# Optimization experiments

Measured on AMD Instinct MI355X. Metric: run time of the kernel, lower is better.

The kernel has to match this reference:

```python
import jax, jax.numpy as jnp
import numpy as np

EPS = 1e-08

def setup_inputs() -> dict:
    key = jax.random.key(0)
    k1, k2, k3, k4 = jax.random.split(key, 4)
    B, T, D, D_sample = 16, 512, 2048, 4096
    z_hist = jax.random.normal(k1, (B, T, D), dtype=jnp.float32)
    decay_rates = jax.random.normal(k2, (D_sample,), dtype=jnp.float32)
    idx_i = jax.random.randint(k3, (D_sample,), 0, D)
    idx_j = jax.random.randint(k4, (D_sample,), 0, D)
    return {"z_hist": z_hist, "decay_rates": decay_rates, "idx_i": idx_i, "idx_j": idx_j}

def reference(z_hist, decay_rates, idx_i, idx_j):
    B, T, D = z_hist.shape
    r = jax.nn.softplus(decay_rates)                      # [N]
    times = jnp.arange(T, dtype=z_hist.dtype)             # [T]
    # decay[t, n] = exp(-r_n * (T - 1 - t))
    decay = jnp.exp(-r[None, :] * (T - 1 - times)[:, None])  # [T, N]
    z_i = z_hist[:, :, idx_i]                              # [B, T, N]
    z_j = z_hist[:, :, idx_j]                              # [B, T, N]
    num = jnp.einsum('btn,btn,tn->bn', z_i, z_j, decay)    # [B, N]
    den = jnp.sqrt(decay.sum(axis=0) + EPS)                # [N]
    return num / den[None, :]
```

## Files before the change

### kernel.cpp

```cpp
#include <hip/hip_runtime.h>
#include <hip/hip_bf16.h>
#include <math.h>

#define B_   16
#define T_   512
#define D_   2048
#define DS_  4096
#define TCHUNK 8
#define EPS_ 1e-8f


__global__ __launch_bounds__(256) void pre_kernel(const float* __restrict__ decay_rates,
                                                  float* __restrict__ num,
                                                  float* __restrict__ inv_den,
                                                  float* __restrict__ neg_r,
                                                  float* __restrict__ er) {
    int gtid = blockIdx.x * 256 + threadIdx.x;
    num[gtid] = 0.f;
    if (gtid < DS_) {
        float x = decay_rates[gtid];
        float r  = (x > 20.f) ? x : log1pf(expf(x));
        float nr = -r;
        float s = 0.f;
        for (int k = 0; k < T_; ++k) s += expf(nr * (float)k);
        inv_den[gtid] = 1.0f / sqrtf(s + EPS_);
        neg_r[gtid]   = nr;
        er[gtid]      = expf(r);
    }
}

__global__ __launch_bounds__(256) void main_kernel(const float* __restrict__ z,
                                                   const int* __restrict__ idx_i,
                                                   const int* __restrict__ idx_j,
                                                   const float* __restrict__ neg_r,
                                                   const float* __restrict__ er,
                                                   float* __restrict__ num) {
    __shared__ float rows[TCHUNK * D_];
    const int tc  = blockIdx.x;
    const int b   = blockIdx.y;
    const int tid = threadIdx.x;

    const float4* src4 = reinterpret_cast<const float4*>(z + ((size_t)b * T_ + (size_t)tc * TCHUNK) * D_);
    float4* lds4 = reinterpret_cast<float4*>(rows);
    #pragma unroll
    for (int v = 0; v < (TCHUNK * D_ / 4) / 256; ++v)
        lds4[tid + v * 256] = src4[tid + v * 256];
    __syncthreads();

    const int kbase = (T_ - 1) - tc * TCHUNK;

    #pragma unroll 1
    for (int s = 0; s < DS_ / 256; ++s) {
        const int n  = tid + s * 256;
        const int ii = idx_i[n];
        const int jj = idx_j[n];
        float w = __expf(neg_r[n] * (float)kbase);
        const float g = er[n];
        float acc = 0.f;
        #pragma unroll
        for (int tl = 0; tl < TCHUNK; ++tl) {
            acc += rows[tl * D_ + ii] * rows[tl * D_ + jj] * w;
            w *= g;
        }
        atomicAdd(&num[b * DS_ + n], acc);
    }
}

__global__ __launch_bounds__(256) void fin_kernel(const float* __restrict__ num,
                                                  const float* __restrict__ inv_den,
                                                  float* __restrict__ out) {
    int gtid = blockIdx.x * 256 + threadIdx.x;
    out[gtid] = num[gtid] * inv_den[gtid & (DS_ - 1)];
}

extern "C" void kernel_launch(void* const* d_in, const int* in_sizes, int n_in,
                              void* d_out, int out_size, void* d_ws, size_t ws_size,
                              hipStream_t stream) {
    const float* z  = (const float*)d_in[0];
    const float* dr = (const float*)d_in[1];
    const int*   ii = (const int*)d_in[2];
    const int*   jj = (const int*)d_in[3];
    float* out = (float*)d_out;

    float* num     = (float*)d_ws;
    float* inv_den = num + B_ * DS_;
    float* neg_r   = inv_den + DS_;
    float* er      = neg_r + DS_;

    hipLaunchKernelGGL(pre_kernel, dim3((B_ * DS_) / 256), dim3(256), 0, stream,
                       dr, num, inv_den, neg_r, er);
    hipLaunchKernelGGL(main_kernel, dim3(T_ / TCHUNK, B_), dim3(256), 0, stream,
                       z, ii, jj, neg_r, er, num);
    hipLaunchKernelGGL(fin_kernel, dim3((B_ * DS_) / 256), dim3(256), 0, stream,
                       num, inv_den, out);
}
```

Measured before the change: 137.1 us.

## Transpose time chunk into float4 LDS quads, halve TCHUNK, closed-form decay sum

```diff
diff --git a/kernel.cpp b/kernel.cpp
--- a/kernel.cpp
+++ b/kernel.cpp
@@ -6,7 +6,7 @@
 #define T_   512
 #define D_   2048
 #define DS_  4096
-#define TCHUNK 8
+#define TCHUNK 4
 #define EPS_ 1e-8f
 
 
@@ -19,49 +19,50 @@
     num[gtid] = 0.f;
     if (gtid < DS_) {
         float x = decay_rates[gtid];
-        float r  = (x > 20.f) ? x : log1pf(expf(x));
-        float nr = -r;
-        float s = 0.f;
-        for (int k = 0; k < T_; ++k) s += expf(nr * (float)k);
-        inv_den[gtid] = 1.0f / sqrtf(s + EPS_);
-        neg_r[gtid]   = nr;
+        float r = (x > 20.f) ? x : log1pf(expf(x));
+        float S = expm1f(-r * (float)T_) / expm1f(-r);
+        inv_den[gtid] = 1.0f / sqrtf(S + EPS_);
+        neg_r[gtid]   = -r;
         er[gtid]      = expf(r);
     }
 }
 
-__global__ __launch_bounds__(256) void main_kernel(const float* __restrict__ z,
-                                                   const int* __restrict__ idx_i,
-                                                   const int* __restrict__ idx_j,
-                                                   const float* __restrict__ neg_r,
-                                                   const float* __restrict__ er,
-                                                   float* __restrict__ num) {
-    __shared__ float rows[TCHUNK * D_];
+__global__ __launch_bounds__(256, 5) void main_kernel(const float* __restrict__ z,
+                                                      const int* __restrict__ idx_i,
+                                                      const int* __restrict__ idx_j,
+                                                      const float* __restrict__ neg_r,
+                                                      const float* __restrict__ er,
+                                                      float* __restrict__ num) {
+    __shared__ float4 quads[D_];
     const int tc  = blockIdx.x;
     const int b   = blockIdx.y;
     const int tid = threadIdx.x;
+    const int t0  = tc * TCHUNK;
+    const float* base = z + ((size_t)b * T_ + t0) * D_;
 
-    const float4* src4 = reinterpret_cast<const float4*>(z + ((size_t)b * T_ + (size_t)tc * TCHUNK) * D_);
-    float4* lds4 = reinterpret_cast<float4*>(rows);
     #pragma unroll
-    for (int v = 0; v < (TCHUNK * D_ / 4) / 256; ++v)
-        lds4[tid + v * 256] = src4[tid + v * 256];
+    for (int it = 0; it < D_ / 256; ++it) {
+        int c = tid + it * 256;
+        quads[c] = make_float4(base[c], base[D_ + c], base[2 * D_ + c], base[3 * D_ + c]);
+    }
     __syncthreads();
 
-    const int kbase = (T_ - 1) - tc * TCHUNK;
+    const int kbase = (T_ - 1) - t0;
 
     #pragma unroll 1
     for (int s = 0; s < DS_ / 256; ++s) {
         const int n  = tid + s * 256;
         const int ii = idx_i[n];
         const int jj = idx_j[n];
-        float w = __expf(neg_r[n] * (float)kbase);
         const float g = er[n];
-        float acc = 0.f;
-        #pragma unroll
-        for (int tl = 0; tl < TCHUNK; ++tl) {
-            acc += rows[tl * D_ + ii] * rows[tl * D_ + jj] * w;
-            w *= g;
-        }
+        const float w0 = __expf(neg_r[n] * (float)kbase);
+        float4 vi = quads[ii];
+        float4 vj = quads[jj];
+        float p0 = vi.x * vj.x;
+        float p1 = vi.y * vj.y;
+        float p2 = vi.z * vj.z;
+        float p3 = vi.w * vj.w;
+        float acc = w0 * (p0 + g * (p1 + g * (p2 + g * p3)));
         atomicAdd(&num[b * DS_ + n], acc);
     }
 }
```

Result: no change. 135.4 us (-1.2%).
